# Performance work log

Hardware: AMD Instinct MI355X
Metric: run time of the kernel (lower is better)

## Reference

```python
import jax, jax.numpy as jnp
import numpy as np

N_NODES = 100000
N_EDGES = 3200000


def gcn_conv(x, edge_index, W, b, n):
    # PyG GCNConv: h = x @ W; add self-loops; symmetric deg normalization; scatter-add; + bias
    src = edge_index[0]
    dst = edge_index[1]
    loop = jnp.arange(n, dtype=src.dtype)
    src = jnp.concatenate([src, loop])
    dst = jnp.concatenate([dst, loop])
    ones = jnp.ones(src.shape[0], dtype=x.dtype)
    deg = jax.ops.segment_sum(ones, dst, num_segments=n)  # in-degree with self-loops
    dinv = jnp.where(deg > 0, jax.lax.rsqrt(deg), 0.0)
    norm = dinv[src] * dinv[dst]  # [E+N]
    h = x @ W  # [N, out]
    msg = h[src] * norm[:, None]
    out = jax.ops.segment_sum(msg, dst, num_segments=n)
    return out + b


def setup_inputs() -> dict:
    key = jax.random.key(0)
    ks = jax.random.split(key, 8)
    x = jax.random.normal(ks[0], (N_NODES, 1024), dtype=jnp.float32)
    edge_index = jax.random.randint(ks[1], (2, N_EDGES), 0, N_NODES, dtype=jnp.int32)
    def glorot(k, fan_in, fan_out):
        s = jnp.sqrt(6.0 / (fan_in + fan_out))
        return jax.random.uniform(k, (fan_in, fan_out), jnp.float32, -s, s)
    W1 = glorot(ks[2], 1024, 128)
    W2 = glorot(ks[3], 128, 128)
    W3 = glorot(ks[4], 128, 9)
    b1 = jnp.zeros((128,), jnp.float32)
    b2 = jnp.zeros((128,), jnp.float32)
    b3 = jnp.zeros((9,), jnp.float32)
    return {"x": x, "edge_index": edge_index, "W1": W1, "b1": b1, "W2": W2, "b2": b2, "W3": W3, "b3": b3}


def reference(x, edge_index, W1, b1, W2, b2, W3, b3):
    n = x.shape[0]
    h = jax.nn.relu(gcn_conv(x, edge_index, W1, b1, n))
    h = jax.nn.relu(gcn_conv(h, edge_index, W2, b2, n))
    h = gcn_conv(h, edge_index, W3, b3, n)
    return jax.nn.log_softmax(h, axis=1)
```

## Files before the change

### kernel.cpp

```cpp
#include <hip/hip_runtime.h>
#include <hip/hip_bf16.h>

typedef __attribute__((ext_vector_type(8))) short bf16x8;
typedef __attribute__((ext_vector_type(4))) float f32x4;

#define BSH 8
#define BNODES 256
#define BCAP 16384

__device__ __forceinline__ unsigned short f2bf(float f) {
    union { float f; unsigned int u; } x; x.f = f;
    unsigned int u = x.u;
    unsigned int r = (u + 0x7fffu + ((u >> 16) & 1u)) >> 16;
    return (unsigned short)r;
}
__device__ __forceinline__ float bf_lo(unsigned int v) { return __uint_as_float(v << 16); }
__device__ __forceinline__ float bf_hi(unsigned int v) { return __uint_as_float(v & 0xffff0000u); }

__device__ __forceinline__ void gll16(const void* g, void* l) {
    __builtin_amdgcn_global_load_lds(
        (const __attribute__((address_space(1))) unsigned int*)g,
        (__attribute__((address_space(3))) unsigned int*)l, 16, 0, 0);
}

template <int N> __device__ __forceinline__ void waitvm() {
    if constexpr (N == 0) asm volatile("s_waitcnt vmcnt(0)" ::: "memory");
    else if constexpr (N == 4) asm volatile("s_waitcnt vmcnt(4)" ::: "memory");
    else if constexpr (N == 6) asm volatile("s_waitcnt vmcnt(6)" ::: "memory");
    else static_assert(N == 0, "unhandled vmcnt");
}


__global__ void k_zero(int* p, int n) {
    int i = blockIdx.x * 256 + threadIdx.x;
    if (i < n) p[i] = 0;
}

#define TPE 16
__global__ __launch_bounds__(256) void kA_scatter(const int* __restrict__ src,
                                                  const int* __restrict__ dst,
                                                  int* gcur, unsigned int* pairs,
                                                  int E, int nbkt) {
    __shared__ int hist[512];
    __shared__ int base[512];
    const int tid = threadIdx.x;
    const int t0 = blockIdx.x * (256 * TPE);
    for (int i = tid; i < 512; i += 256) hist[i] = 0;
    __syncthreads();

    int es[TPE], ed[TPE], rk[TPE];
    bool valid[TPE];
    if (t0 + 256 * TPE <= E) {
        const int4* s4 = (const int4*)(src + t0 + tid * TPE);
        const int4* d4 = (const int4*)(dst + t0 + tid * TPE);
#pragma unroll
        for (int j = 0; j < TPE / 4; j++) {
            int4 a = s4[j], b = d4[j];
            es[4 * j + 0] = a.x; es[4 * j + 1] = a.y; es[4 * j + 2] = a.z; es[4 * j + 3] = a.w;
            ed[4 * j + 0] = b.x; ed[4 * j + 1] = b.y; ed[4 * j + 2] = b.z; ed[4 * j + 3] = b.w;
            valid[4 * j + 0] = valid[4 * j + 1] = valid[4 * j + 2] = valid[4 * j + 3] = true;
        }
    } else {
#pragma unroll
        for (int j = 0; j < TPE; j++) {
            int e = t0 + tid * TPE + j;
            valid[j] = (e < E);
            es[j] = valid[j] ? src[e] : 0;
            ed[j] = valid[j] ? dst[e] : 0;
        }
    }
#pragma unroll
    for (int j = 0; j < TPE; j++)
        if (valid[j]) rk[j] = atomicAdd(&hist[ed[j] >> BSH], 1);
    __syncthreads();
    for (int i = tid; i < nbkt; i += 256) {
        int c = hist[i];
        base[i] = c ? atomicAdd(&gcur[i], c) : 0;
    }
    __syncthreads();
#pragma unroll
    for (int j = 0; j < TPE; j++) {
        if (valid[j]) {
            int b = ed[j] >> BSH;
            int pos = base[b] + rk[j];
            if (pos < BCAP) {
                unsigned int p = ((unsigned int)(ed[j] & (BNODES - 1)) << 24) | (unsigned int)es[j];
                pairs[(size_t)b * BCAP + pos] = p;
            }
        }
    }
}

__global__ __launch_bounds__(512) void kB_group(const unsigned int* __restrict__ pairs,
                                                const int* __restrict__ gcur,
                                                int* csr, int* offs, int* cnt, float* dinv,
                                                int N, int nbkt) {
    int b = blockIdx.x;
    int p0 = b * BCAP;
    int psz = min(gcur[b], BCAP);
    int node0 = b << BSH;
    int nn = min(BNODES, N - node0);
    __shared__ int lcnt[BNODES];
    __shared__ int ss[BNODES];
    __shared__ int lcur[BNODES];
    int t = threadIdx.x;
    if (t < BNODES) lcnt[t] = 0;
    __syncthreads();
    for (int i = t; i < psz; i += 512)
        atomicAdd(&lcnt[pairs[p0 + i] >> 24], 1);
    __syncthreads();
    int v = (t < BNODES) ? lcnt[t] : 0;
    if (t < BNODES) ss[t] = v;
    __syncthreads();
    for (int o = 1; o < BNODES; o <<= 1) {
        int x = (t >= o && t < BNODES) ? ss[t - o] : 0;
        __syncthreads();
        if (t < BNODES) ss[t] += x;
        __syncthreads();
    }
    if (t < nn) {
        int o = p0 + ss[t] - v;
        offs[node0 + t] = o;
        cnt[node0 + t] = v;
        dinv[node0 + t] = rsqrtf((float)(v + 1));
        lcur[t] = o;
    }
    __syncthreads();
    for (int i = t; i < psz; i += 512) {
        unsigned int p = pairs[p0 + i];
        int pos = atomicAdd(&lcur[p >> 24], 1);
        csr[pos] = (int)(p & 0xFFFFFFu);
    }
}

__global__ void k_wt2(const float* __restrict__ W1, unsigned short* w1t,
                      const float* __restrict__ W2, unsigned short* w2t) {
    int i = blockIdx.x * 256 + threadIdx.x;
    if (i < 1024 * 128) {
        int k = i >> 7, c = i & 127;
        w1t[c * 1024 + k] = f2bf(W1[i]);
    } else {
        int j = i - 1024 * 128;
        if (j < 128 * 128) {
            int k = j >> 7, c = j & 127;
            w2t[c * 128 + k] = f2bf(W2[j]);
        }
    }
}


template <int K, bool IN_F32>
__global__ __launch_bounds__(256) void k_gemm(const void* __restrict__ Xv,
                                              const unsigned short* __restrict__ Wt,
                                              const float* __restrict__ dinv,
                                              unsigned short* __restrict__ G, int M) {
    constexpr int ABYTES = IN_F32 ? 128 * 32 * 4 : 128 * 32 * 2;
    constexpr int BBYTES = 128 * 32 * 2;
    constexpr int NT = K / 32;
    constexpr int NBUF = 3;
    constexpr int L = IN_F32 ? 6 : 4;
    static_assert(NT >= 3, "pipeline needs >=3 tiles");
    __shared__ char smem[NBUF * (ABYTES + BBYTES)];

    const int tid = threadIdx.x;
    const int m0 = blockIdx.x * 128;
    const int w = tid >> 6, l = tid & 63, r = l & 15, kg = l >> 4;
    const int wb0 = tid & ~63;

    auto stage = [&](int buf, int k0) {
        if (IN_F32) {
            const float* X = (const float*)Xv;
            char* ab = smem + buf * ABYTES;
#pragma unroll
            for (int i = 0; i < 4; i++) {
                int wb = i * 256 + wb0;
                int c = wb + l;
                int row = c >> 3, slot = c & 7;
                int g = (slot - (row & 7)) & 7;
                int srow = m0 + row; if (srow >= M) srow = M - 1;
                gll16(X + (size_t)srow * K + k0 + g * 4, ab + (size_t)wb * 16);
            }
        } else {
            const unsigned short* X = (const unsigned short*)Xv;
            char* ab = smem + buf * ABYTES;
#pragma unroll
            for (int i = 0; i < 2; i++) {
                int wb = i * 256 + wb0;
                int c = wb + l;
                int row = c >> 2, slot = c & 3;
                int g = (slot - (row >> 2)) & 3;
                int srow = m0 + row; if (srow >= M) srow = M - 1;
                gll16(X + (size_t)srow * K + k0 + g * 8, ab + (size_t)wb * 16);
            }
        }
        {
            char* bb = smem + NBUF * ABYTES + buf * BBYTES;
#pragma unroll
            for (int i = 0; i < 2; i++) {
                int wb = i * 256 + wb0;
                int c = wb + l;
                int row = c >> 2, slot = c & 3;
                int g = (slot - (row >> 2)) & 3;
                gll16(Wt + (size_t)row * K + k0 + g * 8, bb + (size_t)wb * 16);
            }
        }
    };

    f32x4 acc[2][8];
#pragma unroll
    for (int mt = 0; mt < 2; mt++)
#pragma unroll
        for (int ct = 0; ct < 8; ct++) acc[mt][ct] = (f32x4){0.f, 0.f, 0.f, 0.f};

    auto compute = [&](int buf) {
        bf16x8 af[2], bfr[8];
        if (IN_F32) {
            const float* ab = (const float*)(smem + buf * ABYTES);
#pragma unroll
            for (int mt = 0; mt < 2; mt++) {
                int row = w * 32 + mt * 16 + r;
                int p = row & 7;
                int s0 = (2 * kg + p) & 7, s1 = (2 * kg + 1 + p) & 7;
                float4 f0 = *(const float4*)(ab + row * 32 + s0 * 4);
                float4 f1 = *(const float4*)(ab + row * 32 + s1 * 4);
                union { bf16x8 v; unsigned short u[8]; } a;
                a.u[0] = f2bf(f0.x); a.u[1] = f2bf(f0.y); a.u[2] = f2bf(f0.z); a.u[3] = f2bf(f0.w);
                a.u[4] = f2bf(f1.x); a.u[5] = f2bf(f1.y); a.u[6] = f2bf(f1.z); a.u[7] = f2bf(f1.w);
                af[mt] = a.v;
            }
        } else {
            const unsigned short* ab = (const unsigned short*)(smem + buf * ABYTES);
#pragma unroll
            for (int mt = 0; mt < 2; mt++) {
                int row = w * 32 + mt * 16 + r;
                int s = (kg + (row >> 2)) & 3;
                af[mt] = *(const bf16x8*)(ab + row * 32 + s * 8);
            }
        }
        {
            const unsigned short* bb = (const unsigned short*)(smem + NBUF * ABYTES + buf * BBYTES);
#pragma unroll
            for (int ct = 0; ct < 8; ct++) {
                int rowb = ct * 16 + r;
                int s = (kg + (rowb >> 2)) & 3;
                bfr[ct] = *(const bf16x8*)(bb + rowb * 32 + s * 8);
            }
        }
#pragma unroll
        for (int mt = 0; mt < 2; mt++)
#pragma unroll
            for (int ct = 0; ct < 8; ct++)
                acc[mt][ct] = __builtin_amdgcn_mfma_f32_16x16x32_bf16(af[mt], bfr[ct], acc[mt][ct], 0, 0, 0);
    };

    stage(0, 0);
    stage(1, 32);

    int cur = 0;
    for (int t = 0; t < NT - 2; ++t) {
        int nb = cur + 2; if (nb >= NBUF) nb -= NBUF;
        waitvm<L>();
        __builtin_amdgcn_s_barrier();
        stage(nb, (t + 2) * 32);
        compute(cur);
        cur = (cur + 1 == NBUF) ? 0 : cur + 1;
    }
    waitvm<L>();
    __builtin_amdgcn_s_barrier();
    compute(cur);
    cur = (cur + 1 == NBUF) ? 0 : cur + 1;
    waitvm<0>();
    __builtin_amdgcn_s_barrier();
    compute(cur);

#pragma unroll
    for (int mt = 0; mt < 2; mt++) {
        int rbase = m0 + w * 32 + mt * 16 + kg * 4;
        float dv[4];
#pragma unroll
        for (int q = 0; q < 4; q++) dv[q] = (rbase + q < M) ? dinv[rbase + q] : 0.f;
#pragma unroll
        for (int ct = 0; ct < 8; ct++) {
#pragma unroll
            for (int q = 0; q < 4; q++) {
                int gr = rbase + q;
                if (gr < M) G[(size_t)gr * 128 + ct * 16 + r] = f2bf(acc[mt][ct][q] * dv[q]);
            }
        }
    }
}


__global__ __launch_bounds__(256) void k_gemm3(const unsigned short* X3, const float* W3,
                                               const float* dinv, unsigned short* G3, int M) {
    __shared__ unsigned short sx[128 * 136];
    __shared__ float sw[128 * 9];
    int tid = threadIdx.x;
    int m0 = blockIdx.x * 128;
#pragma unroll
    for (int p = 0; p < 8; p++) {
        int idx = p * 256 + tid;
        int row = idx >> 4, c8 = idx & 15;
        uint4 v = make_uint4(0u, 0u, 0u, 0u);
        if (m0 + row < M) v = *(const uint4*)(X3 + (size_t)(m0 + row) * 128 + c8 * 8);
        *(uint4*)&sx[row * 136 + c8 * 8] = v;
    }
    for (int i = tid; i < 128 * 9; i += 256) sw[i] = W3[i];
    __syncthreads();

    int r = tid >> 1, h = tid & 1;
    float acc[9];
#pragma unroll
    for (int c = 0; c < 9; c++) acc[c] = 0.f;
    for (int kk = 0; kk < 64; kk++) {
        int k = h * 64 + kk;
        float xv = __uint_as_float(((unsigned int)sx[r * 136 + k]) << 16);
#pragma unroll
        for (int c = 0; c < 9; c++) acc[c] += xv * sw[k * 9 + c];
    }
#pragma unroll
    for (int c = 0; c < 9; c++) acc[c] += __shfl_xor(acc[c], 1);
    int gr = m0 + r;
    if (h == 0 && gr < M) {
        float dv = dinv[gr];
#pragma unroll
        for (int c = 0; c < 9; c++) G3[(size_t)gr * 16 + c] = f2bf(acc[c] * dv);
#pragma unroll
        for (int c = 9; c < 16; c++) G3[(size_t)gr * 16 + c] = 0;
    }
}


#define A128_CAP 1024

__global__ __launch_bounds__(256) void k_agg128(const unsigned int* __restrict__ gv,
                                                const int* __restrict__ csr,
                                                const int* __restrict__ offs,
                                                const int* __restrict__ cnt,
                                                const float* __restrict__ dinv,
                                                const float* __restrict__ bias,
                                                unsigned int* xout, int N, int do_relu) {
    __shared__ int sidx[A128_CAP];
    const int tid = threadIdx.x;
    const int n0 = blockIdx.x * 4;
    const int nlast = min(n0 + 3, N - 1);
    const int base = offs[n0];
    const int tot = offs[nlast] + cnt[nlast] - base;
    const bool lds_ok = (tot <= A128_CAP);
    if (lds_ok)
        for (int i = tid; i < tot; i += 256) sidx[i] = csr[base + i];
    __syncthreads();

    const int node = n0 + (tid >> 6);
    if (node >= N) return;
    const int l = tid & 63;
    const int ne = cnt[node];
    const int st = offs[node] - base;

    unsigned int u = gv[node * 64 + l];
    float a0 = bf_lo(u), a1 = bf_hi(u);
    int e = 0;
    if (lds_ok) {
        for (; e + 8 <= ne; e += 8) {
            int s0 = sidx[st + e], s1 = sidx[st + e + 1];
            int s2 = sidx[st + e + 2], s3 = sidx[st + e + 3];
            int s4 = sidx[st + e + 4], s5 = sidx[st + e + 5];
            int s6 = sidx[st + e + 6], s7 = sidx[st + e + 7];
            unsigned int v0 = gv[s0 * 64 + l], v1 = gv[s1 * 64 + l];
            unsigned int v2 = gv[s2 * 64 + l], v3 = gv[s3 * 64 + l];
            unsigned int v4 = gv[s4 * 64 + l], v5 = gv[s5 * 64 + l];
            unsigned int v6 = gv[s6 * 64 + l], v7 = gv[s7 * 64 + l];
            a0 += bf_lo(v0); a1 += bf_hi(v0);
            a0 += bf_lo(v1); a1 += bf_hi(v1);
            a0 += bf_lo(v2); a1 += bf_hi(v2);
            a0 += bf_lo(v3); a1 += bf_hi(v3);
            a0 += bf_lo(v4); a1 += bf_hi(v4);
            a0 += bf_lo(v5); a1 += bf_hi(v5);
            a0 += bf_lo(v6); a1 += bf_hi(v6);
            a0 += bf_lo(v7); a1 += bf_hi(v7);
        }
        for (; e < ne; e++) {
            unsigned int v = gv[sidx[st + e] * 64 + l];
            a0 += bf_lo(v); a1 += bf_hi(v);
        }
    } else {
        const int gst = offs[node];
        for (; e < ne; e++) {
            unsigned int v = gv[csr[gst + e] * 64 + l];
            a0 += bf_lo(v); a1 += bf_hi(v);
        }
    }
    float dv = dinv[node];
    float o0 = fmaf(dv, a0, bias[2 * l]);
    float o1 = fmaf(dv, a1, bias[2 * l + 1]);
    if (do_relu) { o0 = fmaxf(o0, 0.f); o1 = fmaxf(o1, 0.f); }
    xout[node * 64 + l] = (unsigned int)f2bf(o0) | ((unsigned int)f2bf(o1) << 16);
}


#define A9_CAP 3072

__global__ __launch_bounds__(256) void k_agg9(const unsigned int* __restrict__ g3v,
                                              const int* __restrict__ csr,
                                              const int* __restrict__ offs,
                                              const int* __restrict__ cnt,
                                              const float* __restrict__ dinv,
                                              const float* __restrict__ b3,
                                              float* out, int N) {
    __shared__ int sidx[A9_CAP];
    const int tid = threadIdx.x;
    const int n0 = blockIdx.x * 32;
    const int nlast = min(n0 + 31, N - 1);
    const int base = offs[n0];
    const int tot = offs[nlast] + cnt[nlast] - base;
    const bool lds_ok = (tot <= A9_CAP);
    if (lds_ok)
        for (int i = tid; i < tot; i += 256) sidx[i] = csr[base + i];
    __syncthreads();

    const int node = n0 + (tid >> 3);
    if (node >= N) return;
    const int jl = tid & 7;
    const int ne = cnt[node];

    unsigned int u = g3v[node * 8 + jl];
    float a0 = bf_lo(u), a1 = bf_hi(u);
    int e = 0;
    if (lds_ok) {
        const int st = offs[node] - base;
        for (; e + 4 <= ne; e += 4) {
            int s0 = sidx[st + e], s1 = sidx[st + e + 1];
            int s2 = sidx[st + e + 2], s3 = sidx[st + e + 3];
            unsigned int v0 = g3v[s0 * 8 + jl], v1 = g3v[s1 * 8 + jl];
            unsigned int v2 = g3v[s2 * 8 + jl], v3 = g3v[s3 * 8 + jl];
            a0 += bf_lo(v0); a1 += bf_hi(v0);
            a0 += bf_lo(v1); a1 += bf_hi(v1);
            a0 += bf_lo(v2); a1 += bf_hi(v2);
            a0 += bf_lo(v3); a1 += bf_hi(v3);
        }
        for (; e < ne; e++) {
            unsigned int v = g3v[sidx[st + e] * 8 + jl];
            a0 += bf_lo(v); a1 += bf_hi(v);
        }
    } else {
        const int gst = offs[node];
        for (; e < ne; e++) {
            unsigned int v = g3v[csr[gst + e] * 8 + jl];
            a0 += bf_lo(v); a1 += bf_hi(v);
        }
    }
    float dv = dinv[node];
    int c0 = 2 * jl, c1 = 2 * jl + 1;
    float o0 = (c0 < 9) ? fmaf(dv, a0, b3[c0]) : -INFINITY;
    float o1 = (c1 < 9) ? fmaf(dv, a1, b3[c1]) : -INFINITY;
    float m = fmaxf(o0, o1);
    for (int d = 1; d < 8; d <<= 1) m = fmaxf(m, __shfl_xor(m, d));
    float s = 0.f;
    if (c0 < 9) s += expf(o0 - m);
    if (c1 < 9) s += expf(o1 - m);
    for (int d = 1; d < 8; d <<= 1) s += __shfl_xor(s, d);
    float ls = m + logf(s);
    if (c0 < 9) out[(size_t)node * 9 + c0] = o0 - ls;
    if (c1 < 9) out[(size_t)node * 9 + c1] = o1 - ls;
}


extern "C" void kernel_launch(void* const* d_in, const int* in_sizes, int n_in,
                              void* d_out, int out_size, void* d_ws, size_t ws_size,
                              hipStream_t stream) {
    const float* x = (const float*)d_in[0];
    const int* ei = (const int*)d_in[1];
    const float* W1 = (const float*)d_in[2];
    const float* b1 = (const float*)d_in[3];
    const float* W2 = (const float*)d_in[4];
    const float* b2 = (const float*)d_in[5];
    const float* W3 = (const float*)d_in[6];
    const float* b3 = (const float*)d_in[7];
    float* out = (float*)d_out;

    const int N = in_sizes[0] / 1024;
    const int E = in_sizes[1] / 2;
    const int* src = ei;
    const int* dst = ei + E;
    const int nbkt = (N + BNODES - 1) >> BSH;

    char* ws = (char*)d_ws;
    size_t off = 0;
    auto alloc = [&](size_t bytes) -> char* {
        char* p = ws + off;
        off += (bytes + 255) & ~(size_t)255;
        return p;
    };
    int* cnt = (int*)alloc((size_t)N * 4);
    int* offs = (int*)alloc((size_t)N * 4);
    float* dinv = (float*)alloc((size_t)N * 4);
    int* gcur = (int*)alloc(520 * 4);
    unsigned int* pairs = (unsigned int*)alloc((size_t)nbkt * BCAP * 4);
    int* csr = (int*)alloc((size_t)nbkt * BCAP * 4);
    unsigned short* w1t = (unsigned short*)alloc(128 * 1024 * 2);
    unsigned short* w2t = (unsigned short*)alloc(128 * 128 * 2);
    unsigned short* gbuf = (unsigned short*)alloc((size_t)N * 128 * 2);
    unsigned short* xbuf = (unsigned short*)alloc((size_t)N * 128 * 2);
    unsigned short* g3 = (unsigned short*)alloc((size_t)N * 16 * 2);

    const int MB = (N + 127) / 128;
    const int AB = (N + 3) / 4;
    const int AB9 = (N + 31) / 32;
    const int SB = (E + 256 * TPE - 1) / (256 * TPE);
    const int WB = (1024 * 128 + 128 * 128 + 255) / 256;

    k_zero<<<3, 256, 0, stream>>>(gcur, 520);
    kA_scatter<<<SB, 256, 0, stream>>>(src, dst, gcur, pairs, E, nbkt);
    kB_group<<<nbkt, 512, 0, stream>>>(pairs, gcur, csr, offs, cnt, dinv, N, nbkt);
    k_wt2<<<WB, 256, 0, stream>>>(W1, w1t, W2, w2t);

    k_gemm<1024, true><<<MB, 256, 0, stream>>>((const void*)x, w1t, dinv, gbuf, N);
    k_agg128<<<AB, 256, 0, stream>>>((const unsigned int*)gbuf, csr, offs, cnt, dinv, b1,
                                     (unsigned int*)xbuf, N, 1);
    k_gemm<128, false><<<MB, 256, 0, stream>>>((const void*)xbuf, w2t, dinv, gbuf, N);
    k_agg128<<<AB, 256, 0, stream>>>((const unsigned int*)gbuf, csr, offs, cnt, dinv, b2,
                                     (unsigned int*)xbuf, N, 1);
    k_gemm3<<<MB, 256, 0, stream>>>(xbuf, W3, dinv, g3, N);
    k_agg9<<<AB9, 256, 0, stream>>>((const unsigned int*)g3, csr, offs, cnt, dinv, b3, out, N);
}
```

Measured before the change: 487.5 us.

## Co-schedule layer-1 GEMM with edge scatter and defer source dinv scaling

Layer 1's GEMM no longer depends on dinv. The source-side dinv factor now moves into the first aggregation, which does a per-edge dinv gather and FMA. That frees the big fp32 GEMM to run in the same launch as the edge-bucketing scatter, with even block IDs doing GEMM tiles and odd ones doing scatter chunks, so memory-bound scatter overlaps compute-bound GEMM. The gcur zeroing is merged into the weight-transpose kernel. The cost is an extra random dinv read per edge in aggregation 1 and a larger shared-memory footprint for the scatter blocks.

New measurement: 623.4 us. +27.9%, slower.

```diff
diff --git a/kernel.cpp b/kernel.cpp
--- a/kernel.cpp
+++ b/kernel.cpp
@@ -31,20 +31,37 @@
 }
 
 
-__global__ void k_zero(int* p, int n) {
+__global__ void k_wt2z(const float* __restrict__ W1, unsigned short* w1t,
+                       const float* __restrict__ W2, unsigned short* w2t, int* gcur) {
     int i = blockIdx.x * 256 + threadIdx.x;
-    if (i < n) p[i] = 0;
-}
+    if (i < 520) gcur[i] = 0;
+    if (i < 1024 * 128) {
+        int k = i >> 7, c = i & 127;
+        w1t[c * 1024 + k] = f2bf(W1[i]);
+    } else {
+        int j = i - 1024 * 128;
+        if (j < 128 * 128) {
+            int k = j >> 7, c = j & 127;
+            w2t[c * 128 + k] = f2bf(W2[j]);
+        }
+    }
+}
+
 
 #define TPE 16
-__global__ __launch_bounds__(256) void kA_scatter(const int* __restrict__ src,
-                                                  const int* __restrict__ dst,
-                                                  int* gcur, unsigned int* pairs,
-                                                  int E, int nbkt) {
-    __shared__ int hist[512];
-    __shared__ int base[512];
+#define G1_ABYTES (128 * 32 * 4)
+#define G1_BBYTES (128 * 32 * 2)
+#define G1_NBUF 3
+#define G1_SMEM (G1_NBUF * (G1_ABYTES + G1_BBYTES))
+
+__device__ void scatter_body(int bid, char* smemraw,
+                             const int* __restrict__ src, const int* __restrict__ dst,
+                             int* gcur, unsigned int* pairs, int E, int nbkt) {
+    int* hist = (int*)smemraw;
+    int* base = (int*)smemraw + 512;
     const int tid = threadIdx.x;
-    const int t0 = blockIdx.x * (256 * TPE);
+    const int t0 = bid * (256 * TPE);
+    if (t0 >= E) return;
     for (int i = tid; i < 512; i += 256) hist[i] = 0;
     __syncthreads();
 
@@ -88,6 +105,130 @@
                 pairs[(size_t)b * BCAP + pos] = p;
             }
         }
+    }
+}
+
+__device__ void gemm1_body(int bid, char* smem,
+                           const float* __restrict__ X,
+                           const unsigned short* __restrict__ Wt,
+                           unsigned short* __restrict__ G, int M) {
+    constexpr int K = 1024;
+    constexpr int NT = K / 32;
+    constexpr int L = 6;
+    const int tid = threadIdx.x;
+    const int m0 = bid * 128;
+    if (m0 >= M) return;
+    const int w = tid >> 6, l = tid & 63, r = l & 15, kg = l >> 4;
+    const int wb0 = tid & ~63;
+
+    auto stage = [&](int buf, int k0) {
+        char* ab = smem + buf * G1_ABYTES;
+#pragma unroll
+        for (int i = 0; i < 4; i++) {
+            int wb = i * 256 + wb0;
+            int c = wb + l;
+            int row = c >> 3, slot = c & 7;
+            int g = (slot - (row & 7)) & 7;
+            int srow = m0 + row; if (srow >= M) srow = M - 1;
+            gll16(X + (size_t)srow * K + k0 + g * 4, ab + (size_t)wb * 16);
+        }
+        char* bb = smem + G1_NBUF * G1_ABYTES + buf * G1_BBYTES;
+#pragma unroll
+        for (int i = 0; i < 2; i++) {
+            int wb = i * 256 + wb0;
+            int c = wb + l;
+            int row = c >> 2, slot = c & 3;
+            int g = (slot - (row >> 2)) & 3;
+            gll16(Wt + (size_t)row * K + k0 + g * 8, bb + (size_t)wb * 16);
+        }
+    };
+
+    f32x4 acc[2][8];
+#pragma unroll
+    for (int mt = 0; mt < 2; mt++)
+#pragma unroll
+        for (int ct = 0; ct < 8; ct++) acc[mt][ct] = (f32x4){0.f, 0.f, 0.f, 0.f};
+
+    auto compute = [&](int buf) {
+        bf16x8 af[2], bfr[8];
+        const float* ab = (const float*)(smem + buf * G1_ABYTES);
+#pragma unroll
+        for (int mt = 0; mt < 2; mt++) {
+            int row = w * 32 + mt * 16 + r;
+            int p = row & 7;
+            int s0 = (2 * kg + p) & 7, s1 = (2 * kg + 1 + p) & 7;
+            float4 f0 = *(const float4*)(ab + row * 32 + s0 * 4);
+            float4 f1 = *(const float4*)(ab + row * 32 + s1 * 4);
+            union { bf16x8 v; unsigned short u[8]; } a;
+            a.u[0] = f2bf(f0.x); a.u[1] = f2bf(f0.y); a.u[2] = f2bf(f0.z); a.u[3] = f2bf(f0.w);
+            a.u[4] = f2bf(f1.x); a.u[5] = f2bf(f1.y); a.u[6] = f2bf(f1.z); a.u[7] = f2bf(f1.w);
+            af[mt] = a.v;
+        }
+        const unsigned short* bb = (const unsigned short*)(smem + G1_NBUF * G1_ABYTES + buf * G1_BBYTES);
+#pragma unroll
+        for (int ct = 0; ct < 8; ct++) {
+            int rowb = ct * 16 + r;
+            int s = (kg + (rowb >> 2)) & 3;
+            bfr[ct] = *(const bf16x8*)(bb + rowb * 32 + s * 8);
+        }
+#pragma unroll
+        for (int mt = 0; mt < 2; mt++)
+#pragma unroll
+            for (int ct = 0; ct < 8; ct++)
+                acc[mt][ct] = __builtin_amdgcn_mfma_f32_16x16x32_bf16(af[mt], bfr[ct], acc[mt][ct], 0, 0, 0);
+    };
+
+    stage(0, 0);
+    stage(1, 32);
+
+    int cur = 0;
+    for (int t = 0; t < NT - 2; ++t) {
+        int nb = cur + 2; if (nb >= G1_NBUF) nb -= G1_NBUF;
+        waitvm<L>();
+        __builtin_amdgcn_s_barrier();
+        stage(nb, (t + 2) * 32);
+        compute(cur);
+        cur = (cur + 1 == G1_NBUF) ? 0 : cur + 1;
+    }
+    waitvm<L>();
+    __builtin_amdgcn_s_barrier();
+    compute(cur);
+    cur = (cur + 1 == G1_NBUF) ? 0 : cur + 1;
+    waitvm<0>();
+    __builtin_amdgcn_s_barrier();
+    compute(cur);
+
+#pragma unroll
+    for (int mt = 0; mt < 2; mt++) {
+        int rbase = m0 + w * 32 + mt * 16 + kg * 4;
+#pragma unroll
+        for (int ct = 0; ct < 8; ct++) {
+#pragma unroll
+            for (int q = 0; q < 4; q++) {
+                int gr = rbase + q;
+                if (gr < M) G[(size_t)gr * 128 + ct * 16 + r] = f2bf(acc[mt][ct][q]);
+            }
+        }
+    }
+}
+
+__global__ __launch_bounds__(256) void k_fused1(const float* __restrict__ X,
+                                                const unsigned short* __restrict__ Wt,
+                                                unsigned short* __restrict__ G, int M, int MB,
+                                                const int* __restrict__ src,
+                                                const int* __restrict__ dst,
+                                                int* gcur, unsigned int* pairs,
+                                                int E, int nbkt, int SB) {
+    __shared__ char smem[G1_SMEM];
+    int bid = blockIdx.x;
+    int mn = (MB < SB) ? MB : SB;
+    if (bid < 2 * mn) {
+        if (bid & 1) scatter_body(bid >> 1, smem, src, dst, gcur, pairs, E, nbkt);
+        else gemm1_body(bid >> 1, smem, X, Wt, G, M);
+    } else {
+        int rm = bid - 2 * mn;
+        if (MB > SB) gemm1_body(mn + rm, smem, X, Wt, G, M);
+        else if (SB > MB) scatter_body(mn + rm, smem, src, dst, gcur, pairs, E, nbkt);
     }
 }
 
@@ -133,32 +274,17 @@
     }
 }
 
-__global__ void k_wt2(const float* __restrict__ W1, unsigned short* w1t,
-                      const float* __restrict__ W2, unsigned short* w2t) {
-    int i = blockIdx.x * 256 + threadIdx.x;
-    if (i < 1024 * 128) {
-        int k = i >> 7, c = i & 127;
-        w1t[c * 1024 + k] = f2bf(W1[i]);
-    } else {
-        int j = i - 1024 * 128;
-        if (j < 128 * 128) {
-            int k = j >> 7, c = j & 127;
-            w2t[c * 128 + k] = f2bf(W2[j]);
-        }
-    }
-}
-
-
-template <int K, bool IN_F32>
-__global__ __launch_bounds__(256) void k_gemm(const void* __restrict__ Xv,
+
+template <int K>
+__global__ __launch_bounds__(256) void k_gemm(const unsigned short* __restrict__ X,
                                               const unsigned short* __restrict__ Wt,
                                               const float* __restrict__ dinv,
                                               unsigned short* __restrict__ G, int M) {
-    constexpr int ABYTES = IN_F32 ? 128 * 32 * 4 : 128 * 32 * 2;
+    constexpr int ABYTES = 128 * 32 * 2;
     constexpr int BBYTES = 128 * 32 * 2;
     constexpr int NT = K / 32;
     constexpr int NBUF = 3;
-    constexpr int L = IN_F32 ? 6 : 4;
+    constexpr int L = 4;
     static_assert(NT >= 3, "pipeline needs >=3 tiles");
     __shared__ char smem[NBUF * (ABYTES + BBYTES)];
 
@@ -168,41 +294,24 @@
     const int wb0 = tid & ~63;
 
     auto stage = [&](int buf, int k0) {
-        if (IN_F32) {
-            const float* X = (const float*)Xv;
-            char* ab = smem + buf * ABYTES;
-#pragma unroll
-            for (int i = 0; i < 4; i++) {
-                int wb = i * 256 + wb0;
-                int c = wb + l;
-                int row = c >> 3, slot = c & 7;
-                int g = (slot - (row & 7)) & 7;
-                int srow = m0 + row; if (srow >= M) srow = M - 1;
-                gll16(X + (size_t)srow * K + k0 + g * 4, ab + (size_t)wb * 16);
-            }
-        } else {
-            const unsigned short* X = (const unsigned short*)Xv;
-            char* ab = smem + buf * ABYTES;
-#pragma unroll
-            for (int i = 0; i < 2; i++) {
-                int wb = i * 256 + wb0;
-                int c = wb + l;
-                int row = c >> 2, slot = c & 3;
-                int g = (slot - (row >> 2)) & 3;
-                int srow = m0 + row; if (srow >= M) srow = M - 1;
-                gll16(X + (size_t)srow * K + k0 + g * 8, ab + (size_t)wb * 16);
-            }
-        }
-        {
-            char* bb = smem + NBUF * ABYTES + buf * BBYTES;
-#pragma unroll
-            for (int i = 0; i < 2; i++) {
-                int wb = i * 256 + wb0;
-                int c = wb + l;
-                int row = c >> 2, slot = c & 3;
-                int g = (slot - (row >> 2)) & 3;
-                gll16(Wt + (size_t)row * K + k0 + g * 8, bb + (size_t)wb * 16);
-            }
+        char* ab = smem + buf * ABYTES;
+#pragma unroll
+        for (int i = 0; i < 2; i++) {
+            int wb = i * 256 + wb0;
+            int c = wb + l;
+            int row = c >> 2, slot = c & 3;
+            int g = (slot - (row >> 2)) & 3;
+            int srow = m0 + row; if (srow >= M) srow = M - 1;
+            gll16(X + (size_t)srow * K + k0 + g * 8, ab + (size_t)wb * 16);
+        }
+        char* bb = smem + NBUF * ABYTES + buf * BBYTES;
+#pragma unroll
+        for (int i = 0; i < 2; i++) {
+            int wb = i * 256 + wb0;
+            int c = wb + l;
+            int row = c >> 2, slot = c & 3;
+            int g = (slot - (row >> 2)) & 3;
+            gll16(Wt + (size_t)row * K + k0 + g * 8, bb + (size_t)wb * 16);
         }
     };
 
@@ -214,37 +323,19 @@
 
     auto compute = [&](int buf) {
         bf16x8 af[2], bfr[8];
-        if (IN_F32) {
-            const float* ab = (const float*)(smem + buf * ABYTES);
-#pragma unroll
-            for (int mt = 0; mt < 2; mt++) {
-                int row = w * 32 + mt * 16 + r;
-                int p = row & 7;
-                int s0 = (2 * kg + p) & 7, s1 = (2 * kg + 1 + p) & 7;
-                float4 f0 = *(const float4*)(ab + row * 32 + s0 * 4);
-                float4 f1 = *(const float4*)(ab + row * 32 + s1 * 4);
-                union { bf16x8 v; unsigned short u[8]; } a;
-                a.u[0] = f2bf(f0.x); a.u[1] = f2bf(f0.y); a.u[2] = f2bf(f0.z); a.u[3] = f2bf(f0.w);
-                a.u[4] = f2bf(f1.x); a.u[5] = f2bf(f1.y); a.u[6] = f2bf(f1.z); a.u[7] = f2bf(f1.w);
-                af[mt] = a.v;
-            }
-        } else {
-            const unsigned short* ab = (const unsigned short*)(smem + buf * ABYTES);
-#pragma unroll
-            for (int mt = 0; mt < 2; mt++) {
-                int row = w * 32 + mt * 16 + r;
-                int s = (kg + (row >> 2)) & 3;
-                af[mt] = *(const bf16x8*)(ab + row * 32 + s * 8);
-            }
-        }
-        {
-            const unsigned short* bb = (const unsigned short*)(smem + NBUF * ABYTES + buf * BBYTES);
-#pragma unroll
-            for (int ct = 0; ct < 8; ct++) {
-                int rowb = ct * 16 + r;
-                int s = (kg + (rowb >> 2)) & 3;
-                bfr[ct] = *(const bf16x8*)(bb + rowb * 32 + s * 8);
-            }
+        const unsigned short* ab = (const unsigned short*)(smem + buf * ABYTES);
+#pragma unroll
+        for (int mt = 0; mt < 2; mt++) {
+            int row = w * 32 + mt * 16 + r;
+            int s = (kg + (row >> 2)) & 3;
+            af[mt] = *(const bf16x8*)(ab + row * 32 + s * 8);
+        }
+        const unsigned short* bb = (const unsigned short*)(smem + NBUF * ABYTES + buf * BBYTES);
+#pragma unroll
+        for (int ct = 0; ct < 8; ct++) {
+            int rowb = ct * 16 + r;
+            int s = (kg + (rowb >> 2)) & 3;
+            bfr[ct] = *(const bf16x8*)(bb + rowb * 32 + s * 8);
         }
 #pragma unroll
         for (int mt = 0; mt < 2; mt++)
@@ -333,6 +424,7 @@
 
 #define A128_CAP 1024
 
+template <int SRC_DINV>
 __global__ __launch_bounds__(256) void k_agg128(const unsigned int* __restrict__ gv,
                                                 const int* __restrict__ csr,
                                                 const int* __restrict__ offs,
@@ -356,9 +448,11 @@
     const int l = tid & 63;
     const int ne = cnt[node];
     const int st = offs[node] - base;
+    const float dv = dinv[node];
+    const float selfs = SRC_DINV ? dv : 1.0f;
 
     unsigned int u = gv[node * 64 + l];
-    float a0 = bf_lo(u), a1 = bf_hi(u);
+    float a0 = bf_lo(u) * selfs, a1 = bf_hi(u) * selfs;
     int e = 0;
     if (lds_ok) {
         for (; e + 8 <= ne; e += 8) {
@@ -370,27 +464,43 @@
             unsigned int v2 = gv[s2 * 64 + l], v3 = gv[s3 * 64 + l];
             unsigned int v4 = gv[s4 * 64 + l], v5 = gv[s5 * 64 + l];
             unsigned int v6 = gv[s6 * 64 + l], v7 = gv[s7 * 64 + l];
-            a0 += bf_lo(v0); a1 += bf_hi(v0);
-            a0 += bf_lo(v1); a1 += bf_hi(v1);
-            a0 += bf_lo(v2); a1 += bf_hi(v2);
-            a0 += bf_lo(v3); a1 += bf_hi(v3);
-            a0 += bf_lo(v4); a1 += bf_hi(v4);
-            a0 += bf_lo(v5); a1 += bf_hi(v5);
-            a0 += bf_lo(v6); a1 += bf_hi(v6);
-            a0 += bf_lo(v7); a1 += bf_hi(v7);
+            if (SRC_DINV) {
+                float d0 = dinv[s0], d1 = dinv[s1], d2 = dinv[s2], d3 = dinv[s3];
+                float d4 = dinv[s4], d5 = dinv[s5], d6 = dinv[s6], d7 = dinv[s7];
+                a0 = fmaf(bf_lo(v0), d0, a0); a1 = fmaf(bf_hi(v0), d0, a1);
+                a0 = fmaf(bf_lo(v1), d1, a0); a1 = fmaf(bf_hi(v1), d1, a1);
+                a0 = fmaf(bf_lo(v2), d2, a0); a1 = fmaf(bf_hi(v2), d2, a1);
+                a0 = fmaf(bf_lo(v3), d3, a0); a1 = fmaf(bf_hi(v3), d3, a1);
+                a0 = fmaf(bf_lo(v4), d4, a0); a1 = fmaf(bf_hi(v4), d4, a1);
+                a0 = fmaf(bf_lo(v5), d5, a0); a1 = fmaf(bf_hi(v5), d5, a1);
+                a0 = fmaf(bf_lo(v6), d6, a0); a1 = fmaf(bf_hi(v6), d6, a1);
+                a0 = fmaf(bf_lo(v7), d7, a0); a1 = fmaf(bf_hi(v7), d7, a1);
+            } else {
+                a0 += bf_lo(v0); a1 += bf_hi(v0);
+                a0 += bf_lo(v1); a1 += bf_hi(v1);
+                a0 += bf_lo(v2); a1 += bf_hi(v2);
+                a0 += bf_lo(v3); a1 += bf_hi(v3);
+                a0 += bf_lo(v4); a1 += bf_hi(v4);
+                a0 += bf_lo(v5); a1 += bf_hi(v5);
+                a0 += bf_lo(v6); a1 += bf_hi(v6);
+                a0 += bf_lo(v7); a1 += bf_hi(v7);
+            }
         }
         for (; e < ne; e++) {
-            unsigned int v = gv[sidx[st + e] * 64 + l];
-            a0 += bf_lo(v); a1 += bf_hi(v);
+            int s = sidx[st + e];
+            unsigned int v = gv[s * 64 + l];
+            float d = SRC_DINV ? dinv[s] : 1.0f;
+            a0 = fmaf(bf_lo(v), d, a0); a1 = fmaf(bf_hi(v), d, a1);
         }
     } else {
         const int gst = offs[node];
         for (; e < ne; e++) {
-            unsigned int v = gv[csr[gst + e] * 64 + l];
-            a0 += bf_lo(v); a1 += bf_hi(v);
-        }
-    }
-    float dv = dinv[node];
+            int s = csr[gst + e];
+            unsigned int v = gv[s * 64 + l];
+            float d = SRC_DINV ? dinv[s] : 1.0f;
+            a0 = fmaf(bf_lo(v), d, a0); a1 = fmaf(bf_hi(v), d, a1);
+        }
+    }
     float o0 = fmaf(dv, a0, bias[2 * l]);
     float o1 = fmaf(dv, a1, bias[2 * l + 1]);
     if (do_relu) { o0 = fmaxf(o0, 0.f); o1 = fmaxf(o1, 0.f); }
@@ -509,17 +619,16 @@
     const int SB = (E + 256 * TPE - 1) / (256 * TPE);
     const int WB = (1024 * 128 + 128 * 128 + 255) / 256;
 
-    k_zero<<<3, 256, 0, stream>>>(gcur, 520);
-    kA_scatter<<<SB, 256, 0, stream>>>(src, dst, gcur, pairs, E, nbkt);
+    k_wt2z<<<WB, 256, 0, stream>>>(W1, w1t, W2, w2t, gcur);
+    k_fused1<<<MB + SB, 256, 0, stream>>>(x, w1t, gbuf, N, MB,
+                                          src, dst, gcur, pairs, E, nbkt, SB);
     kB_group<<<nbkt, 512, 0, stream>>>(pairs, gcur, csr, offs, cnt, dinv, N, nbkt);
-    k_wt2<<<WB, 256, 0, stream>>>(W1, w1t, W2, w2t);
-
-    k_gemm<1024, true><<<MB, 256, 0, stream>>>((const void*)x, w1t, dinv, gbuf, N);
-    k_agg128<<<AB, 256, 0, stream>>>((const unsigned int*)gbuf, csr, offs, cnt, dinv, b1,
-                                     (unsigned int*)xbuf, N, 1);
-    k_gemm<128, false><<<MB, 256, 0, stream>>>((const void*)xbuf, w2t, dinv, gbuf, N);
-    k_agg128<<<AB, 256, 0, stream>>>((const unsigned int*)gbuf, csr, offs, cnt, dinv, b2,
-                                     (unsigned int*)xbuf, N, 1);
+
+    k_agg128<1><<<AB, 256, 0, stream>>>((const unsigned int*)gbuf, csr, offs, cnt, dinv, b1,
+                                        (unsigned int*)xbuf, N, 1);
+    k_gemm<128><<<MB, 256, 0, stream>>>(xbuf, w2t, dinv, gbuf, N);
+    k_agg128<0><<<AB, 256, 0, stream>>>((const unsigned int*)gbuf, csr, offs, cnt, dinv, b2,
+                                        (unsigned int*)xbuf, N, 1);
     k_gemm3<<<MB, 256, 0, stream>>>(xbuf, W3, dinv, g3, N);
     k_agg9<<<AB9, 256, 0, stream>>>((const unsigned int*)g3, csr, offs, cnt, dinv, b3, out, N);
 }
```
